# Kernel optimization log

Hardware: AMD Instinct MI355X
Metric: run time of the kernel (lower is better)

## Reference

```python
import jax, jax.numpy as jnp
import numpy as np

NEG_SLOPE = 0.01  # torch LeakyReLU default

def leaky_relu(x):
    return jnp.where(x >= 0, x, NEG_SLOPE * x)

def gcn_conv(h, W, b, src, dst, n):
    # PyG GCNConv: linear (no bias), add self-loops, symmetric norm, scatter-add, + bias
    h = h @ W  # [N, F]
    loop = jnp.arange(n, dtype=src.dtype)
    s = jnp.concatenate([src, loop])
    d = jnp.concatenate([dst, loop])
    deg = jax.ops.segment_sum(jnp.ones_like(d, dtype=h.dtype), d, num_segments=n)
    dinv = jnp.where(deg > 0, deg ** -0.5, 0.0)
    norm = dinv[s] * dinv[d]  # [E+N]
    msg = h[s] * norm[:, None]
    out = jax.ops.segment_sum(msg, d, num_segments=n)
    return out + b

def setup_inputs() -> dict:
    key = jax.random.key(0)
    ks = jax.random.split(key, 12)
    N, E, D_IN, D_H, D_OUT, C = 100000, 3200000, 512, 128, 64, 2
    def lin(k, fi, fo):
        bound = 1.0 / np.sqrt(fi)
        k1, k2 = jax.random.split(k)
        W = jax.random.uniform(k1, (fi, fo), jnp.float32, -bound, bound)
        b = jax.random.uniform(k2, (fo,), jnp.float32, -bound, bound)
        return W, b
    W1, b1 = lin(ks[0], D_IN, D_H)
    W2, b2 = lin(ks[1], D_H, D_OUT)
    Wg1, bg1 = lin(ks[2], D_OUT, D_OUT)
    Wg2, bg2 = lin(ks[3], D_OUT, D_OUT)
    Wc, bc = lin(ks[4], D_OUT, C)
    x = jax.random.normal(ks[5], (N, D_IN), jnp.float32)
    edge_index = jax.random.randint(ks[6], (2, E), 0, N, jnp.int32)
    return {"x": x, "edge_index": edge_index, "W1": W1, "b1": b1, "W2": W2, "b2": b2,
            "Wg1": Wg1, "bg1": bg1, "Wg2": Wg2, "bg2": bg2, "Wc": Wc, "bc": bc}

def reference(x, edge_index, W1, b1, W2, b2, Wg1, bg1, Wg2, bg2, Wc, bc):
    n = x.shape[0]
    src, dst = edge_index[0], edge_index[1]
    # encoder (dropout = identity in eval)
    h = leaky_relu(x @ W1 + b1)
    h = leaky_relu(h @ W2 + b2)
    # two GCN layers
    h = leaky_relu(gcn_conv(h, Wg1, bg1, src, dst, n))
    h = leaky_relu(gcn_conv(h, Wg2, bg2, src, dst, n))
    logits = h @ Wc + bc
    return logits, h
```

## Files before the change

### kernel.cpp

```cpp
#include <hip/hip_runtime.h>
#include <hip/hip_bf16.h>

typedef __bf16 v8bf16 __attribute__((ext_vector_type(8)));
typedef float  v4f32  __attribute__((ext_vector_type(4)));
typedef unsigned short ushort8v __attribute__((ext_vector_type(8)));

static __device__ __forceinline__ float leaky(float v) { return v >= 0.0f ? v : 0.01f * v; }
static __device__ __forceinline__ float bfbits2f(unsigned short b) {
    union { unsigned u; float f; } c; c.u = ((unsigned)b) << 16; return c.f;
}
static __device__ __forceinline__ unsigned short f2bfbits(float f) {
    __hip_bfloat16 h = __float2bfloat16(f);
    unsigned short s; __builtin_memcpy(&s, &h, 2); return s;
}

constexpr int EPB  = 6400;
constexpr int BCAP = 16384;

static __device__ __forceinline__ bool role_split(int bid, int nA, int tot,
                                                  int& idxA, int& idxB) {
    const long long s0 = (long long)bid * nA / tot;
    const long long s1 = (long long)(bid + 1) * nA / tot;
    if (s1 > s0) { idxA = (int)s0; idxB = 0; return true; }
    idxA = 0; idxB = bid - (int)s0; return false;
}

__global__ __launch_bounds__(256) void prep_all(
    const float* __restrict__ W1, const float* __restrict__ W2,
    const float* __restrict__ Wg1, const float* __restrict__ Wg2,
    __hip_bfloat16* __restrict__ W1f, __hip_bfloat16* __restrict__ W2t,
    __hip_bfloat16* __restrict__ Wg1t, __hip_bfloat16* __restrict__ Wg2t,
    unsigned* __restrict__ bcur, int DIN, int DH, int DO, int NB) {
    const int fragTotal  = DIN * DH;
    const int fragBlocks = (fragTotal + 255) / 256;
    const int n2 = DH * DO, ng = DO * DO;
    const int smallTotal  = n2 + 2 * ng;
    const int smallBlocks = (smallTotal + 255) / 256;
    const int bid = blockIdx.x;
    if (bid < fragBlocks) {
        int tid = bid * 256 + threadIdx.x;
        if (tid >= fragTotal) return;
        int j = tid & 7, l = (tid >> 3) & 63, G = tid >> 9;
        int m = l & 15, q = l >> 4;
        int t = G & 7, kk = G >> 3;
        int n = t * 16 + m;
        int k = kk * 32 + q * 8 + j;
        W1f[tid] = __float2bfloat16(W1[k * DH + n]);
    } else if (bid < fragBlocks + smallBlocks) {
        int i = (bid - fragBlocks) * 256 + threadIdx.x;
        if (i < n2) {
            int r = i / DO, c = i % DO;
            W2t[c * DH + r] = __float2bfloat16(W2[i]);
        } else if (i < n2 + ng) {
            int j = i - n2; int r = j / DO, c = j % DO;
            Wg1t[c * DO + r] = __float2bfloat16(Wg1[j]);
        } else if (i < smallTotal) {
            int j = i - n2 - ng; int r = j / DO, c = j % DO;
            Wg2t[c * DO + r] = __float2bfloat16(Wg2[j]);
        }
    } else {
        int i = (bid - fragBlocks - smallBlocks) * 256 + threadIdx.x;
        if (i < NB) bcur[i] = 0u;
    }
}

struct ScatterSmem {
    unsigned stg[EPB];
    unsigned hist[512], inc[512], cur[512], start[512];
};

static __device__ __forceinline__ void scatter_body(
    int bid, ScatterSmem& sm, const int* __restrict__ src, const int* __restrict__ dst,
    unsigned* __restrict__ bcur, unsigned* __restrict__ ebuck, int E, int NB) {
    const int tid = threadIdx.x;
    sm.hist[tid] = 0u;
    __syncthreads();
    const int beg = bid * EPB;
    const int end = min(beg + EPB, E);
    unsigned myd[13];
#pragma unroll
    for (int i = 0; i < 13; i++) {
        const int e = beg + tid + i * 512;
        if (e < end) {
            const unsigned d = (unsigned)dst[e];
            myd[i] = d;
            atomicAdd(&sm.hist[d >> 8], 1u);
        }
    }
    __syncthreads();
    const unsigned h = sm.hist[tid];
    sm.inc[tid] = h;
    __syncthreads();
    for (int off = 1; off < 512; off <<= 1) {
        unsigned t = (tid >= off) ? sm.inc[tid - off] : 0u;
        __syncthreads();
        sm.inc[tid] += t;
        __syncthreads();
    }
    sm.cur[tid] = sm.inc[tid] - h;
    if (tid < NB && h > 0u)
        sm.start[tid] = (unsigned)tid * BCAP + atomicAdd(&bcur[tid], h);
    __syncthreads();
#pragma unroll
    for (int i = 0; i < 13; i++) {
        const int e = beg + tid + i * 512;
        if (e < end) {
            const unsigned b = myd[i] >> 8;
            const unsigned r = atomicAdd(&sm.cur[b], 1u);
            sm.stg[r] = (unsigned)e;
        }
    }
    __syncthreads();
    const int cnt = end - beg;
    for (int s = tid; s < cnt; s += 512) {
        const unsigned e = sm.stg[s];
        const unsigned d = (unsigned)dst[e];
        const unsigned b = d >> 8;
        const unsigned excl = sm.inc[b] - sm.hist[b];
        const unsigned pos = sm.start[b] + ((unsigned)s - excl);
        ebuck[pos] = (unsigned)src[e] | ((d & 255u) << 20);
    }
}

static __device__ __forceinline__ void enc1_body(
    int bid, const float* __restrict__ A, const v8bf16* __restrict__ Bp,
    const float* __restrict__ bias, __hip_bfloat16* __restrict__ C, int M) {
    constexpr int K = 512;
    const int tid = threadIdx.x;
    const int wid = tid >> 6, lane = tid & 63;
    const int m = lane & 15, q = lane >> 4;
    const int row0 = bid * 128 + wid * 16;
    const int rowA = row0 + m;
    const int rowAc = rowA < M ? rowA : M - 1;
    const float* Ap = A + (size_t)rowAc * K + q * 8;

    v4f32 acc[8];
#pragma unroll
    for (int t = 0; t < 8; t++) acc[t] = (v4f32){0.f, 0.f, 0.f, 0.f};

    float4 ab[2][4];
    auto loadA = [&](int c, int par) {
#pragma unroll
        for (int j = 0; j < 4; j++)
            ab[par][j] = *reinterpret_cast<const float4*>(Ap + c * 64 + (j >> 1) * 32 + (j & 1) * 4);
    };

    loadA(0, 0);
#pragma unroll
    for (int c = 0; c < 8; c++) {
        if (c < 7) loadA(c + 1, (c + 1) & 1);
        const int par = c & 1;
#pragma unroll
        for (int kk2 = 0; kk2 < 2; kk2++) {
            float4 f0 = ab[par][kk2 * 2], f1 = ab[par][kk2 * 2 + 1];
            v8bf16 a = {(__bf16)f0.x, (__bf16)f0.y, (__bf16)f0.z, (__bf16)f0.w,
                        (__bf16)f1.x, (__bf16)f1.y, (__bf16)f1.z, (__bf16)f1.w};
#pragma unroll
            for (int t = 0; t < 8; t++) {
                v8bf16 b = Bp[(size_t)(c * 16 + kk2 * 8 + t) * 64 + lane];
                acc[t] = __builtin_amdgcn_mfma_f32_16x16x32_bf16(a, b, acc[t], 0, 0, 0);
            }
        }
    }

#pragma unroll
    for (int r = 0; r < 4; r++) {
        const int row = row0 + q * 4 + r;
        if (row >= M) continue;
#pragma unroll
        for (int t = 0; t < 8; t++) {
            const int col = t * 16 + m;
            C[(size_t)row * 128 + col] = __float2bfloat16(leaky(acc[t][r] + bias[col]));
        }
    }
}

__global__ __launch_bounds__(512, 4) void mega_scatter_enc1(
    const int* __restrict__ src, const int* __restrict__ dst,
    unsigned* __restrict__ bcur, unsigned* __restrict__ ebuck, int E, int NB, int nScatter,
    const float* __restrict__ A, const v8bf16* __restrict__ Bp,
    const float* __restrict__ bias, __hip_bfloat16* __restrict__ C, int M) {
    __shared__ ScatterSmem sm;
    int ia, ib;
    if (role_split(blockIdx.x, nScatter, gridDim.x, ia, ib))
        scatter_body(ia, sm, src, dst, bcur, ebuck, E, NB);
    else
        enc1_body(ib, A, Bp, bias, C, M);
}

template <int NT, int MODE>
static __device__ __forceinline__ void gemm_body(
    int bid, const __hip_bfloat16* __restrict__ A, const __hip_bfloat16* __restrict__ Bt,
    const float* __restrict__ bias, const float* __restrict__ dinv,
    __hip_bfloat16* __restrict__ Cbf, int M, int K) {
    const int wid  = threadIdx.x >> 6;
    const int lane = threadIdx.x & 63;
    const int row0 = (bid * 4 + wid) << 4;
    if (row0 >= M) return;
    const int m = lane & 15, q = lane >> 4;

    const __hip_bfloat16* Ab = A + (size_t)(row0 + m) * K + q * 8;

    v4f32 acc[NT];
#pragma unroll
    for (int t = 0; t < NT; t++) acc[t] = (v4f32){0.f, 0.f, 0.f, 0.f};

    for (int k0 = 0; k0 < K; k0 += 32) {
        v8bf16 a = *reinterpret_cast<const v8bf16*>(Ab + k0);
#pragma unroll
        for (int t = 0; t < NT; t++) {
            v8bf16 b = *reinterpret_cast<const v8bf16*>(Bt + (size_t)(t * 16 + m) * K + k0 + q * 8);
            acc[t] = __builtin_amdgcn_mfma_f32_16x16x32_bf16(a, b, acc[t], 0, 0, 0);
        }
    }

    const int N = NT * 16;
#pragma unroll
    for (int r = 0; r < 4; r++) {
        const int row = row0 + q * 4 + r;
        float di = (MODE == 1) ? dinv[row] : 1.0f;
#pragma unroll
        for (int t = 0; t < NT; t++) {
            const int col = t * 16 + m;
            float v = acc[t][r];
            if (MODE == 0) v = leaky(v + bias[col]);
            else           v *= di;
            Cbf[(size_t)row * N + col] = __float2bfloat16(v);
        }
    }
}

template <int NT, int MODE>
__global__ __launch_bounds__(256) void gemm_kernel(
    const __hip_bfloat16* __restrict__ A, const __hip_bfloat16* __restrict__ Bt,
    const float* __restrict__ bias, const float* __restrict__ dinv,
    __hip_bfloat16* __restrict__ Cbf, int M, int K) {
    gemm_body<NT, MODE>(blockIdx.x, A, Bt, bias, dinv, Cbf, M, K);
}

static __device__ __forceinline__ void csr_body(
    int k, unsigned* hist, unsigned* cur, const unsigned* __restrict__ bcur,
    const unsigned* __restrict__ ebuck, uint2* __restrict__ rp2,
    float* __restrict__ dinv, int* __restrict__ csr, int NN) {
    const int tid = threadIdx.x;
    const unsigned cntb = bcur[k];
    const unsigned base = (unsigned)k * BCAP;
    const unsigned* eb = ebuck + base;
    hist[tid] = 0u;
    __syncthreads();
    for (unsigned e = tid; e < cntb; e += 256)
        atomicAdd(&hist[eb[e] >> 20], 1u);
    __syncthreads();
    const unsigned h = hist[tid];
    cur[tid] = h;
    __syncthreads();
    for (int off = 1; off < 256; off <<= 1) {
        unsigned t = (tid >= off) ? cur[tid - off] : 0u;
        __syncthreads();
        cur[tid] += t;
        __syncthreads();
    }
    const unsigned excl = cur[tid] - h;
    const int node = k * 256 + tid;
    if (node < NN) {
        rp2[node] = make_uint2(base + excl, base + excl + h);
        dinv[node] = rsqrtf((float)(h + 1u));
    }
    __syncthreads();
    cur[tid] = excl;
    __syncthreads();
    for (unsigned e = tid; e < cntb; e += 256) {
        const unsigned pk = eb[e];
        const unsigned pos = base + atomicAdd(&cur[pk >> 20], 1u);
        csr[pos] = (int)(pk & 0xFFFFFu);
    }
}

__global__ __launch_bounds__(256) void mega_csr_enc2(
    const unsigned* __restrict__ bcur, const unsigned* __restrict__ ebuck,
    uint2* __restrict__ rp2, float* __restrict__ dinv, int* __restrict__ csr,
    int NN, int nCsr,
    const __hip_bfloat16* __restrict__ A, const __hip_bfloat16* __restrict__ Bt,
    const float* __restrict__ bias, __hip_bfloat16* __restrict__ Cb, int M, int K) {
    __shared__ unsigned hist[256], cur[256];
    int ia, ib;
    if (role_split(blockIdx.x, nCsr, gridDim.x, ia, ib))
        csr_body(ia, hist, cur, bcur, ebuck, rp2, dinv, csr, NN);
    else
        gemm_body<4, 0>(ib, A, Bt, bias, nullptr, Cb, M, K);
}

template <int HEAD>
__global__ __launch_bounds__(256) void gather_kernel(
    const uint2* __restrict__ rp2, const int* __restrict__ csr_src,
    const __hip_bfloat16* __restrict__ u, const float* __restrict__ dinv,
    const float* __restrict__ bias, __hip_bfloat16* __restrict__ out_bf,
    float* __restrict__ out_h, const float* __restrict__ Wc,
    const float* __restrict__ bc, float* __restrict__ out_logits, int n) {
    const int node = blockIdx.x * 4 + (threadIdx.x >> 6);
    if (node >= n) return;
    const int lane = threadIdx.x & 63;
    const int g = lane >> 3, t = lane & 7;
    const uint2 rp = rp2[node];
    const unsigned beg = rp.x, end = rp.y;

    float s[8];
#pragma unroll
    for (int j = 0; j < 8; j++) s[j] = 0.f;

    unsigned e = beg + g;
    bool hA = e < end, hB = e + 8 < end;
    int sA = hA ? csr_src[e] : 0;
    int sB = hB ? csr_src[e + 8] : 0;
    while (hA) {
        const unsigned en = e + 16;
        const bool hA2 = en < end, hB2 = en + 8 < end;
        const int sA2 = hA2 ? csr_src[en] : 0;
        const int sB2 = hB2 ? csr_src[en + 8] : 0;
        ushort8v wA = *reinterpret_cast<const ushort8v*>(u + (size_t)sA * 64 + t * 8);
        if (hB) {
            ushort8v wB = *reinterpret_cast<const ushort8v*>(u + (size_t)sB * 64 + t * 8);
#pragma unroll
            for (int j = 0; j < 8; j++) s[j] += bfbits2f(wA[j]) + bfbits2f(wB[j]);
        } else {
#pragma unroll
            for (int j = 0; j < 8; j++) s[j] += bfbits2f(wA[j]);
        }
        e = en; hA = hA2; hB = hB2; sA = sA2; sB = sB2;
    }
#pragma unroll
    for (int j = 0; j < 8; j++) {
        s[j] += __shfl_xor(s[j], 8, 64);
        s[j] += __shfl_xor(s[j], 16, 64);
        s[j] += __shfl_xor(s[j], 32, 64);
    }

    ushort8v wsr = *reinterpret_cast<const ushort8v*>(u + (size_t)node * 64 + t * 8);
#pragma unroll
    for (int j = 0; j < 8; j++) s[j] += bfbits2f(wsr[j]);

    const float di = dinv[node];
    const float4 b0 = *reinterpret_cast<const float4*>(bias + t * 8);
    const float4 b1 = *reinterpret_cast<const float4*>(bias + t * 8 + 4);
    float f[8];
    f[0] = leaky(s[0] * di + b0.x); f[1] = leaky(s[1] * di + b0.y);
    f[2] = leaky(s[2] * di + b0.z); f[3] = leaky(s[3] * di + b0.w);
    f[4] = leaky(s[4] * di + b1.x); f[5] = leaky(s[5] * di + b1.y);
    f[6] = leaky(s[6] * di + b1.z); f[7] = leaky(s[7] * di + b1.w);

    if (HEAD == 0) {
        if (g == 0) {
            ushort8v o;
#pragma unroll
            for (int j = 0; j < 8; j++) o[j] = f2bfbits(f[j]);
            *reinterpret_cast<ushort8v*>(out_bf + (size_t)node * 64 + t * 8) = o;
        }
    } else {
        if (g == 0) {
            float4 o0 = {f[0], f[1], f[2], f[3]};
            float4 o1 = {f[4], f[5], f[6], f[7]};
            *reinterpret_cast<float4*>(out_h + (size_t)node * 64 + t * 8) = o0;
            *reinterpret_cast<float4*>(out_h + (size_t)node * 64 + t * 8 + 4) = o1;
        }
        float p0 = 0.f, p1 = 0.f;
#pragma unroll
        for (int j = 0; j < 8; j++) {
            p0 += f[j] * Wc[(t * 8 + j) * 2];
            p1 += f[j] * Wc[(t * 8 + j) * 2 + 1];
        }
#pragma unroll
        for (int o = 4; o; o >>= 1) {
            p0 += __shfl_xor(p0, o, 64);
            p1 += __shfl_xor(p1, o, 64);
        }
        if (lane == 0) {
            out_logits[(size_t)node * 2 + 0] = p0 + bc[0];
            out_logits[(size_t)node * 2 + 1] = p1 + bc[1];
        }
    }
}

extern "C" void kernel_launch(void* const* d_in, const int* in_sizes, int n_in,
                              void* d_out, int out_size, void* d_ws, size_t ws_size,
                              hipStream_t stream) {
    const float* x   = (const float*)d_in[0];
    const int*   ei  = (const int*)d_in[1];
    const float* W1  = (const float*)d_in[2];
    const float* b1  = (const float*)d_in[3];
    const float* W2  = (const float*)d_in[4];
    const float* b2  = (const float*)d_in[5];
    const float* Wg1 = (const float*)d_in[6];
    const float* bg1 = (const float*)d_in[7];
    const float* Wg2 = (const float*)d_in[8];
    const float* bg2 = (const float*)d_in[9];
    const float* Wc  = (const float*)d_in[10];
    const float* bc  = (const float*)d_in[11];

    const int DH  = in_sizes[3];
    const int DIN = in_sizes[2] / DH;
    const int NN  = in_sizes[0] / DIN;
    const int E   = in_sizes[1] / 2;
    const int DO  = in_sizes[5];
    const int* src = ei;
    const int* dst = ei + E;

    char*  ws  = (char*)d_ws;
    size_t off = 0;
    auto alloc = [&](size_t bytes) {
        void* p = ws + off;
        off += (bytes + 255) & ~(size_t)255;
        return p;
    };
    const int NB = (NN + 255) >> 8;
    __hip_bfloat16* h1    = (__hip_bfloat16*)alloc((size_t)NN * DH * 2);
    __hip_bfloat16* h2    = (__hip_bfloat16*)alloc((size_t)NN * DO * 2);
    __hip_bfloat16* h3    = (__hip_bfloat16*)alloc((size_t)NN * DO * 2);
    __hip_bfloat16* ub    = (__hip_bfloat16*)alloc((size_t)NN * DO * 2);
    float*          dinv  = (float*)alloc((size_t)NN * 4);
    uint2*          rp2   = (uint2*)alloc((size_t)NN * 8);
    int*            csr   = (int*)alloc((size_t)NB * BCAP * 4);
    unsigned*       ebuck = (unsigned*)alloc((size_t)NB * BCAP * 4);
    unsigned*       bcur  = (unsigned*)alloc(512 * 4);
    __hip_bfloat16* W1f   = (__hip_bfloat16*)alloc((size_t)DIN * DH * 2);
    __hip_bfloat16* W2t   = (__hip_bfloat16*)alloc((size_t)DH * DO * 2);
    __hip_bfloat16* Wg1t  = (__hip_bfloat16*)alloc((size_t)DO * DO * 2);
    __hip_bfloat16* Wg2t  = (__hip_bfloat16*)alloc((size_t)DO * DO * 2);

    float* out_logits = (float*)d_out;
    float* out_h      = (float*)d_out + (size_t)NN * 2;

    const int fragBlocks  = (DIN * DH + 255) / 256;
    const int smallBlocks = (DH * DO + 2 * DO * DO + 255) / 256;
    const int zeroBlocks  = (NB + 255) / 256;
    prep_all<<<fragBlocks + smallBlocks + zeroBlocks, 256, 0, stream>>>(
        W1, W2, Wg1, Wg2, W1f, W2t, Wg1t, Wg2t, bcur, DIN, DH, DO, NB);

    const int nblkP = (E + EPB - 1) / EPB;
    const int enc1B = (NN + 127) / 128;
    mega_scatter_enc1<<<nblkP + enc1B, 512, 0, stream>>>(
        src, dst, bcur, ebuck, E, NB, nblkP,
        x, (const v8bf16*)W1f, b1, h1, NN);

    const int gemm_blocks = (NN / 16 + 3) / 4;
    mega_csr_enc2<<<NB + gemm_blocks, 256, 0, stream>>>(
        bcur, ebuck, rp2, dinv, csr, NN, NB,
        h1, W2t, b2, h2, NN, DH);

    gemm_kernel<4, 1><<<gemm_blocks, 256, 0, stream>>>(h2, Wg1t, nullptr, dinv, ub, NN, DO);
    gather_kernel<0><<<(NN + 3) / 4, 256, 0, stream>>>(rp2, csr, ub, dinv, bg1, h3,
                                                       nullptr, nullptr, nullptr, nullptr, NN);

    gemm_kernel<4, 1><<<gemm_blocks, 256, 0, stream>>>(h3, Wg2t, nullptr, dinv, ub, NN, DO);
    gather_kernel<1><<<(NN + 3) / 4, 256, 0, stream>>>(rp2, csr, ub, dinv, bg2, nullptr,
                                                       out_h, Wc, bc, out_logits, NN);
}
```

Baseline: 596.5 us.

## Stage encoder weight tiles in LDS and deepen gather prefetch to four edges

The first encoder GEMM now double-buffers each 16KB chunk of the pre-fragmented W1 into shared memory, reusing the scatter kernel's LDS through a union. The eight waves of a block then read weights from LDS instead of each fetching them from global memory. This adds a __syncthreads per K chunk. Separately, the gather loop processes four edges per lane group per iteration with prefetched indices, putting more random row loads in flight at the cost of extra registers.

```diff
diff --git a/kernel.cpp b/kernel.cpp
--- a/kernel.cpp
+++ b/kernel.cpp
@@ -123,7 +123,7 @@
 }
 
 static __device__ __forceinline__ void enc1_body(
-    int bid, const float* __restrict__ A, const v8bf16* __restrict__ Bp,
+    int bid, uint4 (*lds)[1024], const float* __restrict__ A, const uint4* __restrict__ Bp,
     const float* __restrict__ bias, __hip_bfloat16* __restrict__ C, int M) {
     constexpr int K = 512;
     const int tid = threadIdx.x;
@@ -144,11 +144,16 @@
         for (int j = 0; j < 4; j++)
             ab[par][j] = *reinterpret_cast<const float4*>(Ap + c * 64 + (j >> 1) * 32 + (j & 1) * 4);
     };
-
+    auto stage = [&](int c, int par) {
+        lds[par][tid]       = Bp[c * 1024 + tid];
+        lds[par][512 + tid] = Bp[c * 1024 + 512 + tid];
+    };
+
+    stage(0, 0);
     loadA(0, 0);
-#pragma unroll
     for (int c = 0; c < 8; c++) {
-        if (c < 7) loadA(c + 1, (c + 1) & 1);
+        __syncthreads();
+        if (c < 7) { stage(c + 1, (c + 1) & 1); loadA(c + 1, (c + 1) & 1); }
         const int par = c & 1;
 #pragma unroll
         for (int kk2 = 0; kk2 < 2; kk2++) {
@@ -157,7 +162,7 @@
                         (__bf16)f1.x, (__bf16)f1.y, (__bf16)f1.z, (__bf16)f1.w};
 #pragma unroll
             for (int t = 0; t < 8; t++) {
-                v8bf16 b = Bp[(size_t)(c * 16 + kk2 * 8 + t) * 64 + lane];
+                v8bf16 b = reinterpret_cast<const v8bf16*>(lds[par])[(kk2 * 8 + t) * 64 + lane];
                 acc[t] = __builtin_amdgcn_mfma_f32_16x16x32_bf16(a, b, acc[t], 0, 0, 0);
             }
         }
@@ -178,14 +183,18 @@
 __global__ __launch_bounds__(512, 4) void mega_scatter_enc1(
     const int* __restrict__ src, const int* __restrict__ dst,
     unsigned* __restrict__ bcur, unsigned* __restrict__ ebuck, int E, int NB, int nScatter,
-    const float* __restrict__ A, const v8bf16* __restrict__ Bp,
+    const float* __restrict__ A, const uint4* __restrict__ Bp,
     const float* __restrict__ bias, __hip_bfloat16* __restrict__ C, int M) {
-    __shared__ ScatterSmem sm;
+    union Smem {
+        ScatterSmem sc;
+        uint4 g[2][1024];
+    };
+    __shared__ Smem sm;
     int ia, ib;
     if (role_split(blockIdx.x, nScatter, gridDim.x, ia, ib))
-        scatter_body(ia, sm, src, dst, bcur, ebuck, E, NB);
+        scatter_body(ia, sm.sc, src, dst, bcur, ebuck, E, NB);
     else
-        enc1_body(ib, A, Bp, bias, C, M);
+        enc1_body(ib, sm.g, A, Bp, bias, C, M);
 }
 
 template <int NT, int MODE>
@@ -309,24 +318,36 @@
     for (int j = 0; j < 8; j++) s[j] = 0.f;
 
     unsigned e = beg + g;
-    bool hA = e < end, hB = e + 8 < end;
-    int sA = hA ? csr_src[e] : 0;
-    int sB = hB ? csr_src[e + 8] : 0;
-    while (hA) {
-        const unsigned en = e + 16;
-        const bool hA2 = en < end, hB2 = en + 8 < end;
-        const int sA2 = hA2 ? csr_src[en] : 0;
-        const int sB2 = hB2 ? csr_src[en + 8] : 0;
-        ushort8v wA = *reinterpret_cast<const ushort8v*>(u + (size_t)sA * 64 + t * 8);
-        if (hB) {
-            ushort8v wB = *reinterpret_cast<const ushort8v*>(u + (size_t)sB * 64 + t * 8);
-#pragma unroll
-            for (int j = 0; j < 8; j++) s[j] += bfbits2f(wA[j]) + bfbits2f(wB[j]);
-        } else {
-#pragma unroll
-            for (int j = 0; j < 8; j++) s[j] += bfbits2f(wA[j]);
-        }
-        e = en; hA = hA2; hB = hB2; sA = sA2; sB = sB2;
+    bool hv[4];
+    int idx[4];
+#pragma unroll
+    for (int p = 0; p < 4; p++) {
+        const unsigned ep = e + 8u * p;
+        hv[p] = ep < end;
+        idx[p] = hv[p] ? csr_src[ep] : 0;
+    }
+    while (hv[0]) {
+        bool nhv[4];
+        int nidx[4];
+#pragma unroll
+        for (int p = 0; p < 4; p++) {
+            const unsigned ep = e + 32u + 8u * p;
+            nhv[p] = ep < end;
+            nidx[p] = nhv[p] ? csr_src[ep] : 0;
+        }
+        ushort8v w[4];
+#pragma unroll
+        for (int p = 0; p < 4; p++)
+            if (hv[p]) w[p] = *reinterpret_cast<const ushort8v*>(u + (size_t)idx[p] * 64 + t * 8);
+#pragma unroll
+        for (int p = 0; p < 4; p++)
+            if (hv[p]) {
+#pragma unroll
+                for (int j = 0; j < 8; j++) s[j] += bfbits2f(w[p][j]);
+            }
+        e += 32u;
+#pragma unroll
+        for (int p = 0; p < 4; p++) { hv[p] = nhv[p]; idx[p] = nidx[p]; }
     }
 #pragma unroll
     for (int j = 0; j < 8; j++) {
@@ -439,7 +460,7 @@
     const int enc1B = (NN + 127) / 128;
     mega_scatter_enc1<<<nblkP + enc1B, 512, 0, stream>>>(
         src, dst, bcur, ebuck, E, NB, nblkP,
-        x, (const v8bf16*)W1f, b1, h1, NN);
+        x, (const uint4*)W1f, b1, h1, NN);
 
     const int gemm_blocks = (NN / 16 + 3) / 4;
     mega_csr_enc2<<<NB + gemm_blocks, 256, 0, stream>>>(
```

Result: faster. 544.2 us (-8.8%).
